# Kernel optimization log

Hardware: AMD Instinct MI355X
Metric: run time of the kernel (lower is better)

The kernel has to match this reference:

```python
import jax, jax.numpy as jnp
import numpy as np
import math

N_BITS = 8
NUM_GROUPS = 32
NUM_HEADS = 8
EPS = 1e-5


def fake_quant(x):
    # UniformAffineQuantizer: dynamic per-tensor asymmetric 8-bit fake quant
    levels = 2 ** N_BITS - 1
    xmin = jnp.minimum(x.min(), 0.0)
    xmax = jnp.maximum(x.max(), 0.0)
    scale = jnp.maximum((xmax - xmin) / levels, 1e-8)
    zp = jnp.round(-xmin / scale)
    xq = jnp.clip(jnp.round(x / scale) + zp, 0, levels)
    return (xq - zp) * scale


def group_norm(x, w, b):
    # x: (B, C, T)
    B, C, T = x.shape
    xg = x.reshape(B, NUM_GROUPS, C // NUM_GROUPS, T)
    mean = xg.mean(axis=(2, 3), keepdims=True)
    var = xg.var(axis=(2, 3), keepdims=True)
    xg = (xg - mean) * jax.lax.rsqrt(var + EPS)
    return xg.reshape(B, C, T) * w[None, :, None] + b[None, :, None]


def setup_inputs() -> dict:
    key = jax.random.key(0)
    ks = jax.random.split(key, 7)
    C = 512
    x = jax.random.normal(ks[0], (8, C, 32, 32), dtype=jnp.float32)
    gn_w = jnp.ones((C,), jnp.float32)
    gn_b = jnp.zeros((C,), jnp.float32)
    qkv_w = jax.random.normal(ks[1], (3 * C, C), jnp.float32) * (1.0 / math.sqrt(C))
    qkv_b = jax.random.normal(ks[2], (3 * C,), jnp.float32) * 0.01
    proj_w = jax.random.normal(ks[3], (C, C), jnp.float32) * (1.0 / math.sqrt(C))
    proj_b = jax.random.normal(ks[4], (C,), jnp.float32) * 0.01
    return {"x": x, "gn_w": gn_w, "gn_b": gn_b, "qkv_w": qkv_w,
            "qkv_b": qkv_b, "proj_w": proj_w, "proj_b": proj_b}


def reference(x, gn_w, gn_b, qkv_w, qkv_b, proj_w, proj_b):
    b, c, *spatial = x.shape
    T = int(np.prod(spatial))
    xf = x.reshape(b, c, T)                       # (B, C, T)
    h = group_norm(xf, gn_w, gn_b)
    qkv = jnp.einsum('oc,bct->bot', qkv_w, h) + qkv_b[None, :, None]  # (B, 3C, T)
    qkv = qkv.reshape(b * NUM_HEADS, -1, T)       # (B*H, 3*ch, T)
    ch = qkv.shape[1] // 3
    q, k, v = jnp.split(qkv, 3, axis=1)
    q = fake_quant(q)
    k = fake_quant(k)
    v = fake_quant(v)
    scale = 1.0 / math.sqrt(math.sqrt(ch))
    w = jnp.einsum('bct,bcs->bts', q * scale, k * scale)
    w = jax.nn.softmax(w.astype(jnp.float32), axis=-1).astype(q.dtype)
    a = jnp.einsum('bts,bcs->bct', w, v)          # (B*H, ch, T)
    a = a.reshape(b, c, T)
    a = jnp.einsum('oc,bct->bot', proj_w, a) + proj_b[None, :, None]
    return (xf + a).reshape(b, c, *spatial)
```

## Files before the change

### kernel.cpp

```cpp
#include <hip/hip_runtime.h>

typedef __attribute__((ext_vector_type(8))) __bf16 bf16x8;
typedef __attribute__((ext_vector_type(4))) __bf16 bf16x4;
typedef __attribute__((ext_vector_type(4))) float  f32x4;


static constexpr size_t QKV_OFF = 0;
static constexpr size_t HT_OFF  = 50331648;
static constexpr size_t WQ_OFF  = HT_OFF + 8388608;
static constexpr size_t WP_OFF  = WQ_OFF + 1572864;
static constexpr size_t MM_OFF  = WP_OFF + 524288;
static constexpr size_t GST_OFF = MM_OFF + 6144;
static constexpr size_t KI_OFF  = MM_OFF + 8192;
static constexpr size_t VI_OFF  = KI_OFF + 8388608;
static constexpr size_t NEED_NEW = VI_OFF + 8388608;

__device__ __forceinline__ float dqi(float x, float inv_s, float zp) {
    float y = rintf(x * inv_s);
    return fminf(fmaxf(y, -zp), 255.0f - zp);
}
__device__ __forceinline__ f32x4 mfma16(bf16x8 a, bf16x8 b, f32x4 c) {
    return __builtin_amdgcn_mfma_f32_16x16x32_bf16(a, b, c, 0, 0, 0);
}
__device__ __forceinline__ float exp2i(float x) {
    float r;
    asm("v_exp_f32 %0, %1" : "=v"(r) : "v"(x));
    return r;
}
__device__ __forceinline__ void glds16(const __bf16* g, __bf16* l) {
    __builtin_amdgcn_global_load_lds((const __attribute__((address_space(1))) void*)g,
                                     (__attribute__((address_space(3))) void*)l, 16, 0, 0);
}
template <int N> __device__ __forceinline__ void waitv() {
    asm volatile("s_waitcnt vmcnt(%0)" :: "n"(N) : "memory");
}
__device__ __forceinline__ void bar_raw() {
    asm volatile("s_barrier" ::: "memory");
}

__device__ __forceinline__ void red_mm(const float* __restrict__ pmm, int id, int tid,
                                       float* sred, float& mn_out, float& mx_out) {
    float mn = pmm[id * 512 + tid * 2];
    float mx = pmm[id * 512 + tid * 2 + 1];
#pragma unroll
    for (int m = 1; m < 64; m <<= 1) {
        mn = fminf(mn, __shfl_xor(mn, m));
        mx = fmaxf(mx, __shfl_xor(mx, m));
    }
    if ((tid & 63) == 0) { sred[(tid >> 6) * 2] = mn; sred[(tid >> 6) * 2 + 1] = mx; }
    __syncthreads();
    mn = fminf(fminf(sred[0], sred[2]), fminf(sred[4], sred[6]));
    mx = fmaxf(fmaxf(sred[1], sred[3]), fmaxf(sred[5], sred[7]));
    __syncthreads();
    mn_out = fminf(mn, 0.0f);
    mx_out = fmaxf(mx, 0.0f);
}

__device__ __forceinline__ void red_mm8(const float* __restrict__ pmm, int id, int tid,
                                        float* sred, float& mn_out, float& mx_out) {
    int slot = tid & 255;
    float mn = pmm[id * 512 + slot * 2];
    float mx = pmm[id * 512 + slot * 2 + 1];
#pragma unroll
    for (int m = 1; m < 64; m <<= 1) {
        mn = fminf(mn, __shfl_xor(mn, m));
        mx = fmaxf(mx, __shfl_xor(mx, m));
    }
    if ((tid & 63) == 0) { sred[(tid >> 6) * 2] = mn; sred[(tid >> 6) * 2 + 1] = mx; }
    __syncthreads();
    float a = fminf(fminf(sred[0], sred[2]), fminf(sred[4], sred[6]));
    float b = fminf(fminf(sred[8], sred[10]), fminf(sred[12], sred[14]));
    mn = fminf(a, b);
    a = fmaxf(fmaxf(sred[1], sred[3]), fmaxf(sred[5], sred[7]));
    b = fmaxf(fmaxf(sred[9], sred[11]), fmaxf(sred[13], sred[15]));
    mx = fmaxf(a, b);
    __syncthreads();
    mn_out = fminf(mn, 0.0f);
    mx_out = fmaxf(mx, 0.0f);
}

__global__ __launch_bounds__(256) void gnstats(const float* __restrict__ x,
                                               const float* __restrict__ qw,
                                               __bf16* __restrict__ wq,
                                               const float* __restrict__ pw,
                                               __bf16* __restrict__ wp,
                                               float* __restrict__ gst) {
    int bid = blockIdx.x, tid = threadIdx.x;
    if (bid < 1024) {
        if (bid < 768) {
            int i = bid * 256 + tid;
            float4 v = ((const float4*)qw)[i];
            bf16x4 o = {(__bf16)v.x, (__bf16)v.y, (__bf16)v.z, (__bf16)v.w};
            ((bf16x4*)wq)[i] = o;
        } else {
            int i = (bid - 768) * 256 + tid;
            float4 v = ((const float4*)pw)[i];
            bf16x4 o = {(__bf16)v.x, (__bf16)v.y, (__bf16)v.z, (__bf16)v.w};
            ((bf16x4*)wp)[i] = o;
        }
        return;
    }
    int blk = bid - 1024;
    int b = blk >> 5, g = blk & 31;
    const float* xp = x + (size_t)(b * 512 + g * 16) * 1024;

    float sum = 0.f, ss = 0.f;
#pragma unroll
    for (int i = 0; i < 16; ++i) {
        float4 v = *(const float4*)(xp + (size_t)i * 1024 + tid * 4);
        sum += v.x + v.y + v.z + v.w;
        ss  += v.x * v.x + v.y * v.y + v.z * v.z + v.w * v.w;
    }
#pragma unroll
    for (int m = 1; m < 64; m <<= 1) {
        sum += __shfl_xor(sum, m);
        ss  += __shfl_xor(ss, m);
    }
    __shared__ float s1[4], s2[4];
    int wid = tid >> 6;
    if ((tid & 63) == 0) { s1[wid] = sum; s2[wid] = ss; }
    __syncthreads();
    if (tid == 0) {
        sum = s1[0] + s1[1] + s1[2] + s1[3];
        ss  = s2[0] + s2[1] + s2[2] + s2[3];
        float mean = sum * (1.0f / 16384.0f);
        float var  = ss * (1.0f / 16384.0f) - mean * mean;
        gst[blk]       = mean;
        gst[256 + blk] = rsqrtf(var + 1e-5f);
    }
}

__global__ __launch_bounds__(256) void gnapply(const float* __restrict__ x,
                                               const float* __restrict__ w,
                                               const float* __restrict__ bv,
                                               const float* __restrict__ gst,
                                               __bf16* __restrict__ hT) {
    int f = blockIdx.x;
    int b = f & 7, ts = f >> 3;
    int t0 = ts * 32;
    int tid = threadIdx.x;

    __shared__ __bf16 sH[32][520];
    int cl = tid >> 3;
    int tl = (tid & 7) * 4;

#pragma unroll
    for (int ci = 0; ci < 16; ++ci) {
        int c = ci * 32 + cl;
        int g = c >> 4;
        float mean = gst[b * 32 + g];
        float rstd = gst[256 + b * 32 + g];
        float wc = w[c] * rstd, bc = bv[c];
        float4 v = *(const float4*)(x + ((size_t)(b * 512 + c)) * 1024 + t0 + tl);
        sH[tl + 0][c] = (__bf16)((v.x - mean) * wc + bc);
        sH[tl + 1][c] = (__bf16)((v.y - mean) * wc + bc);
        sH[tl + 2][c] = (__bf16)((v.z - mean) * wc + bc);
        sH[tl + 3][c] = (__bf16)((v.w - mean) * wc + bc);
    }
    __syncthreads();
    int lane = tid & 63, wv = tid >> 6;
#pragma unroll
    for (int it = 0; it < 8; ++it) {
        int row = it * 4 + wv;
        bf16x8 o = *(const bf16x8*)&sH[row][lane * 8];
        *(bf16x8*)(hT + ((size_t)(b * 1024 + t0 + row)) * 512 + lane * 8) = o;
    }
}

template <int MTILE, int MOT, bool MINMAX, bool RESID>
__global__ __launch_bounds__(256, 2) void mgemm5(const __bf16* __restrict__ A,
                                                 const __bf16* __restrict__ Bt,
                                                 const float* __restrict__ bias,
                                                 const float* __restrict__ resid,
                                                 float* __restrict__ out,
                                                 int M, float* __restrict__ pmm) {
    constexpr int NF  = (MTILE == 128) ? 4 : 2;
    constexpr int ASZ = MTILE * 64;
    constexpr int BSZ = 128 * 64;
    constexpr int LA  = MTILE / 32;
    constexpr int L   = LA + 4;
    constexpr int STG = 2 * (ASZ + BSZ) * 2;
    constexpr int CSB = 64 * 132 * 4;
    __shared__ __attribute__((aligned(16))) char smem_raw[(STG > CSB) ? STG : CSB];
    __bf16* sA0 = (__bf16*)smem_raw;
    __bf16* sA1 = sA0 + ASZ;
    __bf16* sB0 = sA1 + ASZ;
    __bf16* sB1 = sB0 + BSZ;
    __shared__ float smn[4], smx[4];

    int tid = threadIdx.x;
    int l = tid & 63, w = tid >> 6;
    int lo = l & 15, hi = l >> 4;

    int f = blockIdx.x;
    constexpr int NWG = MOT * 64;
    int wg = (f & 7) * (NWG / 8) + (f >> 3);
    int mo = wg % MOT, nb = wg / MOT;
    int nt = nb & 7, b = nb >> 3;

    const __bf16* Ap = A + (size_t)mo * MTILE * 512;
    const __bf16* Bp = Bt + ((size_t)b * 1024 + (size_t)nt * 128) * 512;
    int m0 = (MTILE == 128) ? (w >> 1) * 64 : 0;
    int n0 = (MTILE == 128) ? (w & 1) * 64 : w * 32;
    f32x4 acc[4][NF] = {};
    int scd = tid & 7;

    auto STAGE = [&](__bf16* dA, __bf16* dB, int k0) {
#pragma unroll
        for (int p = 0; p < LA; ++p) {
            int lin = p * 2048 + tid * 8;
            int row = lin >> 6;
            glds16(Ap + (size_t)row * 512 + k0 + ((scd ^ (row & 7)) << 3), dA + lin);
        }
#pragma unroll
        for (int p = 0; p < 4; ++p) {
            int lin = p * 2048 + tid * 8;
            int row = lin >> 6;
            glds16(Bp + (size_t)row * 512 + k0 + ((scd ^ (row & 7)) << 3), dB + lin);
        }
    };
    auto COMPUTE = [&](const __bf16* cA, const __bf16* cB) {
#pragma unroll
        for (int kk = 0; kk < 2; ++kk) {
            int rch = ((kk * 4 + hi) ^ (lo & 7)) << 3;
            bf16x8 af[4], bfr[NF];
#pragma unroll
            for (int i = 0; i < 4; ++i) af[i] = *(const bf16x8*)&cA[(m0 + 16 * i + lo) * 64 + rch];
#pragma unroll
            for (int j = 0; j < NF; ++j) bfr[j] = *(const bf16x8*)&cB[(n0 + 16 * j + lo) * 64 + rch];
#pragma unroll
            for (int i = 0; i < 4; ++i)
#pragma unroll
                for (int j = 0; j < NF; ++j) acc[i][j] = mfma16(af[i], bfr[j], acc[i][j]);
        }
    };

    STAGE(sA0, sB0, 0);
#pragma unroll
    for (int kp = 0; kp < 8; kp += 2) {
        if (kp + 1 < 8) { STAGE(sA1, sB1, (kp + 1) * 64); waitv<L>(); } else { waitv<0>(); }
        bar_raw();
        COMPUTE(sA0, sB0);
        bar_raw();
        if (kp + 2 < 8) { STAGE(sA0, sB0, (kp + 2) * 64); waitv<L>(); } else { waitv<0>(); }
        bar_raw();
        COMPUTE(sA1, sB1);
        bar_raw();
    }

    float* cs = (float*)smem_raw;
    float mn = 1e30f, mx = -1e30f;
    constexpr int NH = (MTILE == 128) ? 2 : 1;
#pragma unroll
    for (int h = 0; h < NH; ++h) {
        __syncthreads();
        if (MTILE == 64 || (w >> 1) == h) {
#pragma unroll
            for (int i = 0; i < 4; ++i)
#pragma unroll
                for (int r = 0; r < 4; ++r) {
                    int rl = 16 * i + hi * 4 + r;
                    float bi = bias[mo * MTILE + h * 64 + rl];
#pragma unroll
                    for (int j = 0; j < NF; ++j)
                        cs[rl * 132 + n0 + 16 * j + lo] = acc[i][j][r] + bi;
                }
        }
        __syncthreads();
#pragma unroll
        for (int it = 0; it < 8; ++it) {
            int lin = it * 256 + tid;
            int rr = lin >> 5, cc = (lin & 31) << 2;
            float4 v = *(const float4*)&cs[rr * 132 + cc];
            if (MINMAX) {
                mn = fminf(mn, fminf(fminf(v.x, v.y), fminf(v.z, v.w)));
                mx = fmaxf(mx, fmaxf(fmaxf(v.x, v.y), fmaxf(v.z, v.w)));
            }
            int grow = mo * MTILE + h * 64 + rr;
            size_t gaddr = ((size_t)b * M + grow) * 1024 + nt * 128 + cc;
            if (RESID) {
                float4 rv = *(const float4*)&resid[gaddr];
                v.x += rv.x; v.y += rv.y; v.z += rv.z; v.w += rv.w;
            }
            *(float4*)&out[gaddr] = v;
        }
    }

    if (MINMAX) {
#pragma unroll
        for (int msk = 1; msk < 64; msk <<= 1) {
            mn = fminf(mn, __shfl_xor(mn, msk));
            mx = fmaxf(mx, __shfl_xor(mx, msk));
        }
        if (l == 0) { smn[w] = mn; smx[w] = mx; }
        __syncthreads();
        if (tid == 0) {
            mn = fminf(fminf(smn[0], smn[1]), fminf(smn[2], smn[3]));
            mx = fmaxf(fmaxf(smx[0], smx[1]), fmaxf(smx[2], smx[3]));
            int id = mo >> 2;
            int slot = nb * 4 + (mo & 3);
            pmm[id * 512 + slot * 2]     = mn;
            pmm[id * 512 + slot * 2 + 1] = mx;
        }
    }
}

__global__ __launch_bounds__(256) void quant_kv(const float* __restrict__ qkv,
                                                const float* __restrict__ pmm,
                                                __bf16* __restrict__ ki,
                                                __bf16* __restrict__ vi) {
    int f = blockIdx.x;
    int b = f & 7;
    int r2 = f >> 3;
    int hh = r2 & 7, tt = r2 >> 3;
    int bh = b * 8 + hh;
    int t0 = tt * 64;
    const float* kg = qkv + ((size_t)(b * 1536 + hh * 192) + 64) * 1024;
    const float* vg = kg + 65536;
    int tid = threadIdx.x;

    __shared__ float sred[8];
    float mn1, mx1, mn2, mx2;
    red_mm(pmm, 1, tid, sred, mn1, mx1);
    red_mm(pmm, 2, tid, sred, mn2, mx2);
    float ksc = fmaxf((mx1 - mn1) * (1.f / 255.f), 1e-8f), kzp = rintf(-mn1 / ksc);
    float vsc = fmaxf((mx2 - mn2) * (1.f / 255.f), 1e-8f), vzp = rintf(-mn2 / vsc);
    float inv_k = 1.f / ksc, inv_v = 1.f / vsc;

    __shared__ __bf16 sT[64][68];
    int cr = tid >> 4, t4 = tid & 15;
    int s = tid >> 2, c0 = (tid & 3) * 16;

    __bf16* vd = vi + (size_t)bh * 65536;
#pragma unroll
    for (int r = 0; r < 4; ++r) {
        int c = 16 * r + cr;
        float4 v = *(const float4*)(vg + (size_t)c * 1024 + t0 + t4 * 4);
        bf16x4 o = {(__bf16)dqi(v.x, inv_v, vzp), (__bf16)dqi(v.y, inv_v, vzp),
                    (__bf16)dqi(v.z, inv_v, vzp), (__bf16)dqi(v.w, inv_v, vzp)};
        *(bf16x4*)(vd + (size_t)c * 1024 + t0 + t4 * 4) = o;
    }

#pragma unroll
    for (int r = 0; r < 4; ++r) {
        int c = 16 * r + cr;
        float4 v = *(const float4*)(kg + (size_t)c * 1024 + t0 + t4 * 4);
        sT[t4 * 4 + 0][c] = (__bf16)dqi(v.x, inv_k, kzp);
        sT[t4 * 4 + 1][c] = (__bf16)dqi(v.y, inv_k, kzp);
        sT[t4 * 4 + 2][c] = (__bf16)dqi(v.z, inv_k, kzp);
        sT[t4 * 4 + 3][c] = (__bf16)dqi(v.w, inv_k, kzp);
    }
    __syncthreads();
    bf16x8 a0 = *(const bf16x8*)&sT[s][c0];
    bf16x8 a1 = *(const bf16x8*)&sT[s][c0 + 8];
    __bf16* kd = ki + ((size_t)bh * 1024 + t0 + s) * 64 + c0;
    *(bf16x8*)kd = a0;
    *(bf16x8*)(kd + 8) = a1;
}

__global__ __launch_bounds__(512, 4) void attn5(const float* __restrict__ qkv,
                                                const __bf16* __restrict__ ki,
                                                const __bf16* __restrict__ vi,
                                                const float* __restrict__ pmm,
                                                __bf16* __restrict__ aT) {
    int f = blockIdx.x;
    int bh = (f & 7) * 8 + ((f >> 3) & 7);
    int tt = f >> 6;
    int b = bh >> 3, hh = bh & 7;
    int t0 = tt * 128;
    const float* qg = qkv + (size_t)(b * 1536 + hh * 192) * 1024;
    const __bf16* kb = ki + (size_t)bh * 65536;
    const __bf16* vb = vi + (size_t)bh * 65536;
    int tid = threadIdx.x;

    __shared__ float sred[16];
    float mn0, mx0, mn1, mx1, mn2, mx2;
    red_mm8(pmm, 0, tid, sred, mn0, mx0);
    red_mm8(pmm, 1, tid, sred, mn1, mx1);
    red_mm8(pmm, 2, tid, sred, mn2, mx2);
    float qsc = fmaxf((mx0 - mn0) * (1.f / 255.f), 1e-8f), qzp = rintf(-mn0 / qsc);
    float ksc = fmaxf((mx1 - mn1) * (1.f / 255.f), 1e-8f);
    float vsc = fmaxf((mx2 - mn2) * (1.f / 255.f), 1e-8f);
    float inv_q = 1.f / qsc;
    float alpha2 = qsc * ksc * 0.125f * 1.4426950408889634f;
    float thr = 11.5415603f / alpha2;

    __shared__ __bf16 sh[128][72];
    __shared__ __bf16 kS[2][4096];
    __shared__ __bf16 vS[2][4096];
    int l = tid & 63, w = tid >> 6;
    int lo = l & 15, hi = l >> 4;

    int srow = tid >> 3, sc = tid & 7;
    int swz = (sc ^ (srow & 7)) << 3;
    const __bf16* kROW = kb + (size_t)srow * 64;
    const __bf16* vROW = vb + (size_t)srow * 1024;
    int lx = lo & 7;
    int rc0 = (hi ^ lx) << 3;
    int rc1 = ((4 + hi) ^ lx) << 3;

    bf16x8 kr = *(const bf16x8*)(kROW + sc * 8);
    bf16x8 vr = *(const bf16x8*)(vROW + sc * 8);

    {
        int c0 = (tid >> 5) * 4;
        int tl = tid & 31;
#pragma unroll
        for (int r = 0; r < 4; ++r) {
            int t = tl + 32 * r;
            float y0 = dqi(qg[(size_t)(c0 + 0) * 1024 + t0 + t], inv_q, qzp);
            float y1 = dqi(qg[(size_t)(c0 + 1) * 1024 + t0 + t], inv_q, qzp);
            float y2 = dqi(qg[(size_t)(c0 + 2) * 1024 + t0 + t], inv_q, qzp);
            float y3 = dqi(qg[(size_t)(c0 + 3) * 1024 + t0 + t], inv_q, qzp);
            bf16x4 o = {(__bf16)y0, (__bf16)y1, (__bf16)y2, (__bf16)y3};
            *(bf16x4*)&sh[t][c0] = o;
        }
    }
    __syncthreads();
    bf16x8 qf0 = *(const bf16x8*)&sh[16 * w + lo][hi * 8];
    bf16x8 qf1 = *(const bf16x8*)&sh[16 * w + lo][32 + hi * 8];
    *(bf16x8*)(kS[0] + srow * 64 + swz) = kr;
    *(bf16x8*)(vS[0] + srow * 64 + swz) = vr;
    __syncthreads();

    f32x4 acc0 = {}, acc1 = {}, acc2 = {}, acc3 = {};
    float m_run = -1e30f, l_run = 0.f;

    for (int st = 0; st < 16; ++st) {
        const __bf16* kc = kS[st & 1];
        const __bf16* vc = vS[st & 1];
        if (st < 15) {
            kr = *(const bf16x8*)(kROW + (st + 1) * 4096 + sc * 8);
            vr = *(const bf16x8*)(vROW + (st + 1) * 64 + sc * 8);
        }

        f32x4 sf[4] = {};
        __builtin_amdgcn_s_setprio(1);
#pragma unroll
        for (int sm = 0; sm < 4; ++sm)
            sf[sm] = mfma16(*(const bf16x8*)(kc + (16 * sm + lo) * 64 + rc0), qf0, sf[sm]);
#pragma unroll
        for (int sm = 0; sm < 4; ++sm)
            sf[sm] = mfma16(*(const bf16x8*)(kc + (16 * sm + lo) * 64 + rc1), qf1, sf[sm]);
        __builtin_amdgcn_s_setprio(0);

        float tm = -1e30f;
#pragma unroll
        for (int sm = 0; sm < 4; ++sm) {
            float a = fmaxf(sf[sm][0], sf[sm][1]);
            float c = fmaxf(sf[sm][2], sf[sm][3]);
            tm = fmaxf(tm, fmaxf(a, c));
        }
        tm = fmaxf(tm, __shfl_xor(tm, 16));
        tm = fmaxf(tm, __shfl_xor(tm, 32));
        if (!__all(tm <= m_run + thr)) {
            float mnew = fmaxf(m_run, tm);
            float fr = exp2i(alpha2 * (m_run - mnew));
            acc0 *= fr; acc1 *= fr; acc2 *= fr; acc3 *= fr;
            l_run *= fr;
            m_run = mnew;
        }
        float cc = -alpha2 * m_run;
        float ts = 0.f;
#pragma unroll
        for (int sm = 0; sm < 4; ++sm)
#pragma unroll
            for (int r = 0; r < 4; ++r) {
                float p = exp2i(fmaf(sf[sm][r], alpha2, cc));
                sf[sm][r] = p;
                ts += p;
            }
        ts += __shfl_xor(ts, 16);
        ts += __shfl_xor(ts, 32);
        l_run += ts;

#pragma unroll
        for (int sm = 0; sm < 4; ++sm) {
            bf16x4 pb = {(__bf16)sf[sm][0], (__bf16)sf[sm][1], (__bf16)sf[sm][2], (__bf16)sf[sm][3]};
            *(bf16x4*)&sh[16 * w + lo][16 * sm + hi * 4] = pb;
        }
        bf16x8 pf0 = *(const bf16x8*)&sh[16 * w + lo][hi * 8];
        bf16x8 pf1 = *(const bf16x8*)&sh[16 * w + lo][32 + hi * 8];

        __builtin_amdgcn_s_setprio(1);
        acc0 = mfma16(*(const bf16x8*)(vc + (lo) * 64 + rc0), pf0, acc0);
        acc1 = mfma16(*(const bf16x8*)(vc + (16 + lo) * 64 + rc0), pf0, acc1);
        acc2 = mfma16(*(const bf16x8*)(vc + (32 + lo) * 64 + rc0), pf0, acc2);
        acc3 = mfma16(*(const bf16x8*)(vc + (48 + lo) * 64 + rc0), pf0, acc3);
        acc0 = mfma16(*(const bf16x8*)(vc + (lo) * 64 + rc1), pf1, acc0);
        acc1 = mfma16(*(const bf16x8*)(vc + (16 + lo) * 64 + rc1), pf1, acc1);
        acc2 = mfma16(*(const bf16x8*)(vc + (32 + lo) * 64 + rc1), pf1, acc2);
        acc3 = mfma16(*(const bf16x8*)(vc + (48 + lo) * 64 + rc1), pf1, acc3);
        __builtin_amdgcn_s_setprio(0);

        if (st < 15) {
            *(bf16x8*)(kS[(st + 1) & 1] + srow * 64 + swz) = kr;
            *(bf16x8*)(vS[(st + 1) & 1] + srow * 64 + swz) = vr;
        }
        __syncthreads();
    }

    float rl = vsc / l_run;
    {
        bf16x4 o0 = {(__bf16)(acc0[0] * rl), (__bf16)(acc0[1] * rl), (__bf16)(acc0[2] * rl), (__bf16)(acc0[3] * rl)};
        bf16x4 o1 = {(__bf16)(acc1[0] * rl), (__bf16)(acc1[1] * rl), (__bf16)(acc1[2] * rl), (__bf16)(acc1[3] * rl)};
        bf16x4 o2 = {(__bf16)(acc2[0] * rl), (__bf16)(acc2[1] * rl), (__bf16)(acc2[2] * rl), (__bf16)(acc2[3] * rl)};
        bf16x4 o3 = {(__bf16)(acc3[0] * rl), (__bf16)(acc3[1] * rl), (__bf16)(acc3[2] * rl), (__bf16)(acc3[3] * rl)};
        *(bf16x4*)&sh[16 * w + lo][0  + hi * 4] = o0;
        *(bf16x4*)&sh[16 * w + lo][16 + hi * 4] = o1;
        *(bf16x4*)&sh[16 * w + lo][32 + hi * 4] = o2;
        *(bf16x4*)&sh[16 * w + lo][48 + hi * 4] = o3;
    }
    __syncthreads();
    __bf16* ap = aT + ((size_t)b * 1024 + t0 + (tid >> 2)) * 512 + hh * 64;
    bf16x8 v0 = *(const bf16x8*)&sh[tid >> 2][(tid & 3) * 8];
    bf16x8 v1 = *(const bf16x8*)&sh[tid >> 2][32 + (tid & 3) * 8];
    *(bf16x8*)(ap + (tid & 3) * 8) = v0;
    *(bf16x8*)(ap + 32 + (tid & 3) * 8) = v1;
}

__global__ __launch_bounds__(256) void attn_mfma(const float* __restrict__ qkv,
                                                 const float* __restrict__ pmm,
                                                 __bf16* __restrict__ aT) {
    int f = blockIdx.x;
    int bh = (f & 7) * 8 + ((f >> 3) & 7);
    int tt = f >> 6;
    int b = bh >> 3, hh = bh & 7;
    int t0 = tt * 64;
    const float* qg = qkv + (size_t)(b * 1536 + hh * 192) * 1024;
    const float* kg = qg + (size_t)64 * 1024;
    const float* vg = qg + (size_t)128 * 1024;
    int tid = threadIdx.x;

    __shared__ float sred[8];
    float mn0, mx0, mn1, mx1, mn2, mx2;
    red_mm(pmm, 0, tid, sred, mn0, mx0);
    red_mm(pmm, 1, tid, sred, mn1, mx1);
    red_mm(pmm, 2, tid, sred, mn2, mx2);
    float qsc = fmaxf((mx0 - mn0) * (1.f / 255.f), 1e-8f), qzp = rintf(-mn0 / qsc);
    float ksc = fmaxf((mx1 - mn1) * (1.f / 255.f), 1e-8f), kzp = rintf(-mn1 / ksc);
    float vsc = fmaxf((mx2 - mn2) * (1.f / 255.f), 1e-8f), vzp = rintf(-mn2 / vsc);
    float inv_q = 1.f / qsc, inv_k = 1.f / ksc, inv_v = 1.f / vsc;
    float alpha = qsc * ksc * 0.125f;

    __shared__ __bf16 qT[64][72];
    __shared__ __bf16 kT[64][72];
    __shared__ __bf16 vL[64][72];
    __shared__ __bf16 pL[4][16][72];

    int l = tid & 63, w = tid >> 6;
    int lo = l & 15, hi = l >> 4;
    int c0 = (tid >> 4) * 4;
    int tl = tid & 15;

#pragma unroll
    for (int r = 0; r < 4; ++r) {
        int t = tl + 16 * r;
        float y0 = dqi(qg[(size_t)(c0 + 0) * 1024 + t0 + t], inv_q, qzp);
        float y1 = dqi(qg[(size_t)(c0 + 1) * 1024 + t0 + t], inv_q, qzp);
        float y2 = dqi(qg[(size_t)(c0 + 2) * 1024 + t0 + t], inv_q, qzp);
        float y3 = dqi(qg[(size_t)(c0 + 3) * 1024 + t0 + t], inv_q, qzp);
        bf16x4 o = {(__bf16)y0, (__bf16)y1, (__bf16)y2, (__bf16)y3};
        *(bf16x4*)&qT[t][c0] = o;
    }
    __syncthreads();
    bf16x8 qf0 = *(const bf16x8*)&qT[16 * w + lo][hi * 8];
    bf16x8 qf1 = *(const bf16x8*)&qT[16 * w + lo][32 + hi * 8];

    f32x4 acc0 = {}, acc1 = {}, acc2 = {}, acc3 = {};
    float m_run = -1e30f, l_run = 0.f;

    for (int st = 0; st < 16; ++st) {
        int s0 = st * 64;
        __syncthreads();
#pragma unroll
        for (int r = 0; r < 4; ++r) {
            int srow = tl + 16 * r;
            float y0 = dqi(kg[(size_t)(c0 + 0) * 1024 + s0 + srow], inv_k, kzp);
            float y1 = dqi(kg[(size_t)(c0 + 1) * 1024 + s0 + srow], inv_k, kzp);
            float y2 = dqi(kg[(size_t)(c0 + 2) * 1024 + s0 + srow], inv_k, kzp);
            float y3 = dqi(kg[(size_t)(c0 + 3) * 1024 + s0 + srow], inv_k, kzp);
            bf16x4 ok = {(__bf16)y0, (__bf16)y1, (__bf16)y2, (__bf16)y3};
            *(bf16x4*)&kT[srow][c0] = ok;
            int c = (tid >> 4) + 16 * r;
            float4 vv = *(const float4*)(vg + (size_t)c * 1024 + s0 + (tid & 15) * 4);
            bf16x4 ov = {(__bf16)dqi(vv.x, inv_v, vzp), (__bf16)dqi(vv.y, inv_v, vzp),
                         (__bf16)dqi(vv.z, inv_v, vzp), (__bf16)dqi(vv.w, inv_v, vzp)};
            *(bf16x4*)&vL[c][(tid & 15) * 4] = ov;
        }
        __syncthreads();

        f32x4 sf[4] = {};
#pragma unroll
        for (int sm = 0; sm < 4; ++sm)
            sf[sm] = mfma16(*(const bf16x8*)&kT[16 * sm + lo][hi * 8], qf0, sf[sm]);
#pragma unroll
        for (int sm = 0; sm < 4; ++sm)
            sf[sm] = mfma16(*(const bf16x8*)&kT[16 * sm + lo][32 + hi * 8], qf1, sf[sm]);

        float tm = -1e30f;
#pragma unroll
        for (int sm = 0; sm < 4; ++sm)
#pragma unroll
            for (int r = 0; r < 4; ++r) { sf[sm][r] *= alpha; tm = fmaxf(tm, sf[sm][r]); }
        tm = fmaxf(tm, __shfl_xor(tm, 16));
        tm = fmaxf(tm, __shfl_xor(tm, 32));
        float mnew = fmaxf(m_run, tm);
        float ts = 0.f;
#pragma unroll
        for (int sm = 0; sm < 4; ++sm)
#pragma unroll
            for (int r = 0; r < 4; ++r) {
                float p = __expf(sf[sm][r] - mnew);
                sf[sm][r] = p;
                ts += p;
            }
        ts += __shfl_xor(ts, 16);
        ts += __shfl_xor(ts, 32);
        float fr = __expf(m_run - mnew);
        l_run = l_run * fr + ts;
        m_run = mnew;
        acc0 *= fr; acc1 *= fr; acc2 *= fr; acc3 *= fr;

#pragma unroll
        for (int sm = 0; sm < 4; ++sm) {
            bf16x4 pb = {(__bf16)sf[sm][0], (__bf16)sf[sm][1], (__bf16)sf[sm][2], (__bf16)sf[sm][3]};
            *(bf16x4*)&pL[w][lo][16 * sm + hi * 4] = pb;
        }
        bf16x8 pf0 = *(const bf16x8*)&pL[w][lo][hi * 8];
        bf16x8 pf1 = *(const bf16x8*)&pL[w][lo][32 + hi * 8];
        acc0 = mfma16(*(const bf16x8*)&vL[lo][hi * 8], pf0, acc0);
        acc1 = mfma16(*(const bf16x8*)&vL[16 + lo][hi * 8], pf0, acc1);
        acc2 = mfma16(*(const bf16x8*)&vL[32 + lo][hi * 8], pf0, acc2);
        acc3 = mfma16(*(const bf16x8*)&vL[48 + lo][hi * 8], pf0, acc3);
        acc0 = mfma16(*(const bf16x8*)&vL[lo][32 + hi * 8], pf1, acc0);
        acc1 = mfma16(*(const bf16x8*)&vL[16 + lo][32 + hi * 8], pf1, acc1);
        acc2 = mfma16(*(const bf16x8*)&vL[32 + lo][32 + hi * 8], pf1, acc2);
        acc3 = mfma16(*(const bf16x8*)&vL[48 + lo][32 + hi * 8], pf1, acc3);
    }

    float rl = vsc / l_run;
    __syncthreads();
    {
        bf16x4 o0 = {(__bf16)(acc0[0] * rl), (__bf16)(acc0[1] * rl), (__bf16)(acc0[2] * rl), (__bf16)(acc0[3] * rl)};
        bf16x4 o1 = {(__bf16)(acc1[0] * rl), (__bf16)(acc1[1] * rl), (__bf16)(acc1[2] * rl), (__bf16)(acc1[3] * rl)};
        bf16x4 o2 = {(__bf16)(acc2[0] * rl), (__bf16)(acc2[1] * rl), (__bf16)(acc2[2] * rl), (__bf16)(acc2[3] * rl)};
        bf16x4 o3 = {(__bf16)(acc3[0] * rl), (__bf16)(acc3[1] * rl), (__bf16)(acc3[2] * rl), (__bf16)(acc3[3] * rl)};
        *(bf16x4*)&qT[16 * w + lo][0  + hi * 4] = o0;
        *(bf16x4*)&qT[16 * w + lo][16 + hi * 4] = o1;
        *(bf16x4*)&qT[16 * w + lo][32 + hi * 4] = o2;
        *(bf16x4*)&qT[16 * w + lo][48 + hi * 4] = o3;
    }
    __syncthreads();
    __bf16* ap = aT + ((size_t)b * 1024 + t0 + (tid >> 2)) * 512 + hh * 64;
    bf16x8 v0 = *(const bf16x8*)&qT[tid >> 2][(tid & 3) * 8];
    bf16x8 v1 = *(const bf16x8*)&qT[tid >> 2][32 + (tid & 3) * 8];
    *(bf16x8*)(ap + (tid & 3) * 8) = v0;
    *(bf16x8*)(ap + 32 + (tid & 3) * 8) = v1;
}

extern "C" void kernel_launch(void* const* d_in, const int* in_sizes, int n_in,
                              void* d_out, int out_size, void* d_ws, size_t ws_size,
                              hipStream_t stream) {
    const float* x      = (const float*)d_in[0];
    const float* gn_w   = (const float*)d_in[1];
    const float* gn_b   = (const float*)d_in[2];
    const float* qkv_w  = (const float*)d_in[3];
    const float* qkv_b  = (const float*)d_in[4];
    const float* proj_w = (const float*)d_in[5];
    const float* proj_b = (const float*)d_in[6];
    char* ws = (char*)d_ws;
    float*    qkv = (float*)(ws + QKV_OFF);
    __bf16*   hT  = (__bf16*)(ws + HT_OFF);
    __bf16*   wq  = (__bf16*)(ws + WQ_OFF);
    __bf16*   wp  = (__bf16*)(ws + WP_OFF);
    float*    pmm = (float*)(ws + MM_OFF);
    float*    gst = (float*)(ws + GST_OFF);
    __bf16*   ki  = (__bf16*)(ws + KI_OFF);
    __bf16*   vi  = (__bf16*)(ws + VI_OFF);
    float* out = (float*)d_out;

    gnstats<<<1280, 256, 0, stream>>>(x, qkv_w, wq, proj_w, wp, gst);
    gnapply<<<256, 256, 0, stream>>>(x, gn_w, gn_b, gst, hT);
    mgemm5<128, 12, true, false><<<768, 256, 0, stream>>>(wq, hT, qkv_b, nullptr, qkv, 1536, pmm);
    if (ws_size >= NEED_NEW) {
        quant_kv<<<1024, 256, 0, stream>>>(qkv, pmm, ki, vi);
        attn5<<<512, 512, 0, stream>>>(qkv, ki, vi, pmm, hT);
    } else {
        attn_mfma<<<1024, 256, 0, stream>>>(qkv, pmm, hT);
    }
    mgemm5<64, 8, false, true><<<512, 256, 0, stream>>>(wp, hT, proj_b, x, out, 512, nullptr);
}
```

Measured before the change: 93.91 us.

## Switch attention to 32x32x16 MFMA with register-resident P via cross-lane shuffles

```diff
diff --git a/kernel.cpp b/kernel.cpp
--- a/kernel.cpp
+++ b/kernel.cpp
@@ -1,8 +1,9 @@
 #include <hip/hip_runtime.h>
 
-typedef __attribute__((ext_vector_type(8))) __bf16 bf16x8;
-typedef __attribute__((ext_vector_type(4))) __bf16 bf16x4;
-typedef __attribute__((ext_vector_type(4))) float  f32x4;
+typedef __attribute__((ext_vector_type(8)))  __bf16 bf16x8;
+typedef __attribute__((ext_vector_type(4)))  __bf16 bf16x4;
+typedef __attribute__((ext_vector_type(4)))  float  f32x4;
+typedef __attribute__((ext_vector_type(16))) float  f32x16;
 
 
 static constexpr size_t QKV_OFF = 0;
@@ -22,6 +23,9 @@
 __device__ __forceinline__ f32x4 mfma16(bf16x8 a, bf16x8 b, f32x4 c) {
     return __builtin_amdgcn_mfma_f32_16x16x32_bf16(a, b, c, 0, 0, 0);
 }
+__device__ __forceinline__ f32x16 mfma32(bf16x8 a, bf16x8 b, f32x16 c) {
+    return __builtin_amdgcn_mfma_f32_32x32x16_bf16(a, b, c, 0, 0, 0);
+}
 __device__ __forceinline__ float exp2i(float x) {
     float r;
     asm("v_exp_f32 %0, %1" : "=v"(r) : "v"(x));
@@ -37,6 +41,11 @@
 __device__ __forceinline__ void bar_raw() {
     asm volatile("s_barrier" ::: "memory");
 }
+__device__ __forceinline__ unsigned pk2(float a, float b) {
+    union { __bf16 h; unsigned short u; } ua, ub;
+    ua.h = (__bf16)a; ub.h = (__bf16)b;
+    return ((unsigned)ub.u << 16) | (unsigned)ua.u;
+}
 
 __device__ __forceinline__ void red_mm(const float* __restrict__ pmm, int id, int tid,
                                        float* sred, float& mn_out, float& mx_out) {
@@ -51,29 +60,6 @@
     __syncthreads();
     mn = fminf(fminf(sred[0], sred[2]), fminf(sred[4], sred[6]));
     mx = fmaxf(fmaxf(sred[1], sred[3]), fmaxf(sred[5], sred[7]));
-    __syncthreads();
-    mn_out = fminf(mn, 0.0f);
-    mx_out = fmaxf(mx, 0.0f);
-}
-
-__device__ __forceinline__ void red_mm8(const float* __restrict__ pmm, int id, int tid,
-                                        float* sred, float& mn_out, float& mx_out) {
-    int slot = tid & 255;
-    float mn = pmm[id * 512 + slot * 2];
-    float mx = pmm[id * 512 + slot * 2 + 1];
-#pragma unroll
-    for (int m = 1; m < 64; m <<= 1) {
-        mn = fminf(mn, __shfl_xor(mn, m));
-        mx = fmaxf(mx, __shfl_xor(mx, m));
-    }
-    if ((tid & 63) == 0) { sred[(tid >> 6) * 2] = mn; sred[(tid >> 6) * 2 + 1] = mx; }
-    __syncthreads();
-    float a = fminf(fminf(sred[0], sred[2]), fminf(sred[4], sred[6]));
-    float b = fminf(fminf(sred[8], sred[10]), fminf(sred[12], sred[14]));
-    mn = fminf(a, b);
-    a = fmaxf(fmaxf(sred[1], sred[3]), fmaxf(sred[5], sred[7]));
-    b = fmaxf(fmaxf(sred[9], sred[11]), fmaxf(sred[13], sred[15]));
-    mx = fmaxf(a, b);
     __syncthreads();
     mn_out = fminf(mn, 0.0f);
     mx_out = fmaxf(mx, 0.0f);
@@ -358,7 +344,7 @@
     *(bf16x8*)(kd + 8) = a1;
 }
 
-__global__ __launch_bounds__(512, 4) void attn5(const float* __restrict__ qkv,
+__global__ __launch_bounds__(256, 2) void attn6(const float* __restrict__ qkv,
                                                 const __bf16* __restrict__ ki,
                                                 const __bf16* __restrict__ vi,
                                                 const float* __restrict__ pmm,
@@ -373,11 +359,11 @@
     const __bf16* vb = vi + (size_t)bh * 65536;
     int tid = threadIdx.x;
 
-    __shared__ float sred[16];
+    __shared__ float sred[8];
     float mn0, mx0, mn1, mx1, mn2, mx2;
-    red_mm8(pmm, 0, tid, sred, mn0, mx0);
-    red_mm8(pmm, 1, tid, sred, mn1, mx1);
-    red_mm8(pmm, 2, tid, sred, mn2, mx2);
+    red_mm(pmm, 0, tid, sred, mn0, mx0);
+    red_mm(pmm, 1, tid, sred, mn1, mx1);
+    red_mm(pmm, 2, tid, sred, mn2, mx2);
     float qsc = fmaxf((mx0 - mn0) * (1.f / 255.f), 1e-8f), qzp = rintf(-mn0 / qsc);
     float ksc = fmaxf((mx1 - mn1) * (1.f / 255.f), 1e-8f);
     float vsc = fmaxf((mx2 - mn2) * (1.f / 255.f), 1e-8f);
@@ -385,138 +371,150 @@
     float alpha2 = qsc * ksc * 0.125f * 1.4426950408889634f;
     float thr = 11.5415603f / alpha2;
 
-    __shared__ __bf16 sh[128][72];
     __shared__ __bf16 kS[2][4096];
     __shared__ __bf16 vS[2][4096];
+    __shared__ __bf16 sQ[128][72];
+
     int l = tid & 63, w = tid >> 6;
-    int lo = l & 15, hi = l >> 4;
-
-    int srow = tid >> 3, sc = tid & 7;
-    int swz = (sc ^ (srow & 7)) << 3;
+    int lt = l & 31;
+    int h  = l >> 5;
+    int lx = lt & 7;
+
+    int srow = tid >> 2, sc2 = (tid & 3) * 2;
+    int swz0 = (sc2 ^ (srow & 7)) << 3;
+    int swz1 = ((sc2 + 1) ^ (srow & 7)) << 3;
     const __bf16* kROW = kb + (size_t)srow * 64;
     const __bf16* vROW = vb + (size_t)srow * 1024;
-    int lx = lo & 7;
-    int rc0 = (hi ^ lx) << 3;
-    int rc1 = ((4 + hi) ^ lx) << 3;
-
-    bf16x8 kr = *(const bf16x8*)(kROW + sc * 8);
-    bf16x8 vr = *(const bf16x8*)(vROW + sc * 8);
+
+    bf16x8 kr0 = *(const bf16x8*)(kROW + sc2 * 8);
+    bf16x8 kr1 = *(const bf16x8*)(kROW + sc2 * 8 + 8);
+    bf16x8 vr0 = *(const bf16x8*)(vROW + sc2 * 8);
+    bf16x8 vr1 = *(const bf16x8*)(vROW + sc2 * 8 + 8);
 
     {
-        int c0 = (tid >> 5) * 4;
+        int c0 = (tid >> 5) * 8;
         int tl = tid & 31;
 #pragma unroll
         for (int r = 0; r < 4; ++r) {
             int t = tl + 32 * r;
-            float y0 = dqi(qg[(size_t)(c0 + 0) * 1024 + t0 + t], inv_q, qzp);
-            float y1 = dqi(qg[(size_t)(c0 + 1) * 1024 + t0 + t], inv_q, qzp);
-            float y2 = dqi(qg[(size_t)(c0 + 2) * 1024 + t0 + t], inv_q, qzp);
-            float y3 = dqi(qg[(size_t)(c0 + 3) * 1024 + t0 + t], inv_q, qzp);
-            bf16x4 o = {(__bf16)y0, (__bf16)y1, (__bf16)y2, (__bf16)y3};
-            *(bf16x4*)&sh[t][c0] = o;
-        }
-    }
-    __syncthreads();
-    bf16x8 qf0 = *(const bf16x8*)&sh[16 * w + lo][hi * 8];
-    bf16x8 qf1 = *(const bf16x8*)&sh[16 * w + lo][32 + hi * 8];
-    *(bf16x8*)(kS[0] + srow * 64 + swz) = kr;
-    *(bf16x8*)(vS[0] + srow * 64 + swz) = vr;
-    __syncthreads();
-
-    f32x4 acc0 = {}, acc1 = {}, acc2 = {}, acc3 = {};
+            bf16x8 o;
+#pragma unroll
+            for (int j = 0; j < 8; ++j)
+                o[j] = (__bf16)dqi(qg[(size_t)(c0 + j) * 1024 + t0 + t], inv_q, qzp);
+            *(bf16x8*)&sQ[t][c0] = o;
+        }
+    }
+    __syncthreads();
+    bf16x8 qf[4];
+#pragma unroll
+    for (int cs = 0; cs < 4; ++cs)
+        qf[cs] = *(const bf16x8*)&sQ[32 * w + lt][16 * cs + 8 * h];
+    *(bf16x8*)(kS[0] + srow * 64 + swz0) = kr0;
+    *(bf16x8*)(kS[0] + srow * 64 + swz1) = kr1;
+    *(bf16x8*)(vS[0] + srow * 64 + swz0) = vr0;
+    *(bf16x8*)(vS[0] + srow * 64 + swz1) = vr1;
+    __syncthreads();
+
+    int rc[4];
+#pragma unroll
+    for (int i = 0; i < 4; ++i) rc[i] = ((2 * i + h) ^ lx) << 3;
+
+    f32x16 accA = {}, accB = {};
     float m_run = -1e30f, l_run = 0.f;
 
     for (int st = 0; st < 16; ++st) {
         const __bf16* kc = kS[st & 1];
         const __bf16* vc = vS[st & 1];
         if (st < 15) {
-            kr = *(const bf16x8*)(kROW + (st + 1) * 4096 + sc * 8);
-            vr = *(const bf16x8*)(vROW + (st + 1) * 64 + sc * 8);
-        }
-
-        f32x4 sf[4] = {};
+            kr0 = *(const bf16x8*)(kROW + (st + 1) * 4096 + sc2 * 8);
+            kr1 = *(const bf16x8*)(kROW + (st + 1) * 4096 + sc2 * 8 + 8);
+            vr0 = *(const bf16x8*)(vROW + (st + 1) * 64 + sc2 * 8);
+            vr1 = *(const bf16x8*)(vROW + (st + 1) * 64 + sc2 * 8 + 8);
+        }
+
+        f32x16 s0 = {}, s1 = {};
         __builtin_amdgcn_s_setprio(1);
 #pragma unroll
-        for (int sm = 0; sm < 4; ++sm)
-            sf[sm] = mfma16(*(const bf16x8*)(kc + (16 * sm + lo) * 64 + rc0), qf0, sf[sm]);
-#pragma unroll
-        for (int sm = 0; sm < 4; ++sm)
-            sf[sm] = mfma16(*(const bf16x8*)(kc + (16 * sm + lo) * 64 + rc1), qf1, sf[sm]);
+        for (int cs = 0; cs < 4; ++cs) {
+            s0 = mfma32(*(const bf16x8*)(kc + (lt) * 64 + rc[cs]), qf[cs], s0);
+            s1 = mfma32(*(const bf16x8*)(kc + (32 + lt) * 64 + rc[cs]), qf[cs], s1);
+        }
         __builtin_amdgcn_s_setprio(0);
 
         float tm = -1e30f;
 #pragma unroll
-        for (int sm = 0; sm < 4; ++sm) {
-            float a = fmaxf(sf[sm][0], sf[sm][1]);
-            float c = fmaxf(sf[sm][2], sf[sm][3]);
-            tm = fmaxf(tm, fmaxf(a, c));
-        }
-        tm = fmaxf(tm, __shfl_xor(tm, 16));
+        for (int j = 0; j < 16; ++j) tm = fmaxf(tm, fmaxf(s0[j], s1[j]));
         tm = fmaxf(tm, __shfl_xor(tm, 32));
         if (!__all(tm <= m_run + thr)) {
             float mnew = fmaxf(m_run, tm);
             float fr = exp2i(alpha2 * (m_run - mnew));
-            acc0 *= fr; acc1 *= fr; acc2 *= fr; acc3 *= fr;
+#pragma unroll
+            for (int j = 0; j < 16; ++j) { accA[j] *= fr; accB[j] *= fr; }
             l_run *= fr;
             m_run = mnew;
         }
         float cc = -alpha2 * m_run;
         float ts = 0.f;
-#pragma unroll
-        for (int sm = 0; sm < 4; ++sm)
-#pragma unroll
-            for (int r = 0; r < 4; ++r) {
-                float p = exp2i(fmaf(sf[sm][r], alpha2, cc));
-                sf[sm][r] = p;
-                ts += p;
-            }
-        ts += __shfl_xor(ts, 16);
+        float p0[16], p1[16];
+#pragma unroll
+        for (int j = 0; j < 16; ++j) { p0[j] = exp2i(fmaf(s0[j], alpha2, cc)); ts += p0[j]; }
+#pragma unroll
+        for (int j = 0; j < 16; ++j) { p1[j] = exp2i(fmaf(s1[j], alpha2, cc)); ts += p1[j]; }
         ts += __shfl_xor(ts, 32);
         l_run += ts;
 
-#pragma unroll
-        for (int sm = 0; sm < 4; ++sm) {
-            bf16x4 pb = {(__bf16)sf[sm][0], (__bf16)sf[sm][1], (__bf16)sf[sm][2], (__bf16)sf[sm][3]};
-            *(bf16x4*)&sh[16 * w + lo][16 * sm + hi * 4] = pb;
-        }
-        bf16x8 pf0 = *(const bf16x8*)&sh[16 * w + lo][hi * 8];
-        bf16x8 pf1 = *(const bf16x8*)&sh[16 * w + lo][32 + hi * 8];
+        unsigned W0[8], W1[8];
+#pragma unroll
+        for (int r2 = 0; r2 < 8; ++r2) {
+            W0[r2] = pk2(p0[2 * r2], p0[2 * r2 + 1]);
+            W1[r2] = pk2(p1[2 * r2], p1[2 * r2 + 1]);
+        }
 
         __builtin_amdgcn_s_setprio(1);
-        acc0 = mfma16(*(const bf16x8*)(vc + (lo) * 64 + rc0), pf0, acc0);
-        acc1 = mfma16(*(const bf16x8*)(vc + (16 + lo) * 64 + rc0), pf0, acc1);
-        acc2 = mfma16(*(const bf16x8*)(vc + (32 + lo) * 64 + rc0), pf0, acc2);
-        acc3 = mfma16(*(const bf16x8*)(vc + (48 + lo) * 64 + rc0), pf0, acc3);
-        acc0 = mfma16(*(const bf16x8*)(vc + (lo) * 64 + rc1), pf1, acc0);
-        acc1 = mfma16(*(const bf16x8*)(vc + (16 + lo) * 64 + rc1), pf1, acc1);
-        acc2 = mfma16(*(const bf16x8*)(vc + (32 + lo) * 64 + rc1), pf1, acc2);
-        acc3 = mfma16(*(const bf16x8*)(vc + (48 + lo) * 64 + rc1), pf1, acc3);
+#pragma unroll
+        for (int ks = 0; ks < 4; ++ks) {
+            const unsigned* Wsb = (ks >> 1) ? W1 : W0;
+            int jown  = 4 * (ks & 1) + 2 * h;
+            int jsend = 4 * (ks & 1) + 2 * (1 - h);
+            unsigned r0 = (unsigned)__shfl_xor((int)Wsb[jsend], 32);
+            unsigned r1 = (unsigned)__shfl_xor((int)Wsb[jsend + 1], 32);
+            union { unsigned u[4]; bf16x8 v; } pf;
+            pf.u[0] = h ? r0 : Wsb[jown];
+            pf.u[1] = h ? r1 : Wsb[jown + 1];
+            pf.u[2] = h ? Wsb[jown] : r0;
+            pf.u[3] = h ? Wsb[jown + 1] : r1;
+            accA = mfma32(*(const bf16x8*)(vc + (lt) * 64 + rc[ks]), pf.v, accA);
+            accB = mfma32(*(const bf16x8*)(vc + (32 + lt) * 64 + rc[ks]), pf.v, accB);
+        }
         __builtin_amdgcn_s_setprio(0);
 
         if (st < 15) {
-            *(bf16x8*)(kS[(st + 1) & 1] + srow * 64 + swz) = kr;
-            *(bf16x8*)(vS[(st + 1) & 1] + srow * 64 + swz) = vr;
+            *(bf16x8*)(kS[(st + 1) & 1] + srow * 64 + swz0) = kr0;
+            *(bf16x8*)(kS[(st + 1) & 1] + srow * 64 + swz1) = kr1;
+            *(bf16x8*)(vS[(st + 1) & 1] + srow * 64 + swz0) = vr0;
+            *(bf16x8*)(vS[(st + 1) & 1] + srow * 64 + swz1) = vr1;
         }
         __syncthreads();
     }
 
     float rl = vsc / l_run;
-    {
-        bf16x4 o0 = {(__bf16)(acc0[0] * rl), (__bf16)(acc0[1] * rl), (__bf16)(acc0[2] * rl), (__bf16)(acc0[3] * rl)};
-        bf16x4 o1 = {(__bf16)(acc1[0] * rl), (__bf16)(acc1[1] * rl), (__bf16)(acc1[2] * rl), (__bf16)(acc1[3] * rl)};
-        bf16x4 o2 = {(__bf16)(acc2[0] * rl), (__bf16)(acc2[1] * rl), (__bf16)(acc2[2] * rl), (__bf16)(acc2[3] * rl)};
-        bf16x4 o3 = {(__bf16)(acc3[0] * rl), (__bf16)(acc3[1] * rl), (__bf16)(acc3[2] * rl), (__bf16)(acc3[3] * rl)};
-        *(bf16x4*)&sh[16 * w + lo][0  + hi * 4] = o0;
-        *(bf16x4*)&sh[16 * w + lo][16 + hi * 4] = o1;
-        *(bf16x4*)&sh[16 * w + lo][32 + hi * 4] = o2;
-        *(bf16x4*)&sh[16 * w + lo][48 + hi * 4] = o3;
-    }
-    __syncthreads();
-    __bf16* ap = aT + ((size_t)b * 1024 + t0 + (tid >> 2)) * 512 + hh * 64;
-    bf16x8 v0 = *(const bf16x8*)&sh[tid >> 2][(tid & 3) * 8];
-    bf16x8 v1 = *(const bf16x8*)&sh[tid >> 2][32 + (tid & 3) * 8];
-    *(bf16x8*)(ap + (tid & 3) * 8) = v0;
-    *(bf16x8*)(ap + 32 + (tid & 3) * 8) = v1;
+#pragma unroll
+    for (int g = 0; g < 4; ++g) {
+        bf16x4 oA = {(__bf16)(accA[4 * g] * rl), (__bf16)(accA[4 * g + 1] * rl),
+                     (__bf16)(accA[4 * g + 2] * rl), (__bf16)(accA[4 * g + 3] * rl)};
+        bf16x4 oB = {(__bf16)(accB[4 * g] * rl), (__bf16)(accB[4 * g + 1] * rl),
+                     (__bf16)(accB[4 * g + 2] * rl), (__bf16)(accB[4 * g + 3] * rl)};
+        *(bf16x4*)&sQ[32 * w + lt][8 * g + 4 * h] = oA;
+        *(bf16x4*)&sQ[32 * w + lt][32 + 8 * g + 4 * h] = oB;
+    }
+    __syncthreads();
+    int row = tid >> 1, half = tid & 1;
+    __bf16* ap = aT + ((size_t)(b * 1024 + t0 + row)) * 512 + hh * 64 + half * 32;
+#pragma unroll
+    for (int c8 = 0; c8 < 4; ++c8) {
+        bf16x8 o = *(const bf16x8*)&sQ[row][half * 32 + c8 * 8];
+        *(bf16x8*)(ap + c8 * 8) = o;
+    }
 }
 
 __global__ __launch_bounds__(256) void attn_mfma(const float* __restrict__ qkv,
@@ -685,7 +683,7 @@
     mgemm5<128, 12, true, false><<<768, 256, 0, stream>>>(wq, hT, qkv_b, nullptr, qkv, 1536, pmm);
     if (ws_size >= NEED_NEW) {
         quant_kv<<<1024, 256, 0, stream>>>(qkv, pmm, ki, vi);
-        attn5<<<512, 512, 0, stream>>>(qkv, ki, vi, pmm, hT);
+        attn6<<<512, 256, 0, stream>>>(qkv, ki, vi, pmm, hT);
     } else {
         attn_mfma<<<1024, 256, 0, stream>>>(qkv, pmm, hT);
     }
```

After: 112.1 us. 19.4% more time.
